# Optimization experiments

Measured on AMD Instinct MI355X. Metric: run time of the kernel, lower is better.

## Reference

```python
import jax, jax.numpy as jnp
import numpy as np

C = 64; NB_ERB = 32; NB_DF = 96; EMB = 256; KT = 2
LSNR_SCALE = 50.0; LSNR_OFFSET = -15.0

def _conv2d(x, w, b, stride=(1, 1)):
    # NCHW conv; freq padding 1, no temporal padding (causal ring buffer handles time)
    out = jax.lax.conv_general_dilated(
        x, w, window_strides=stride, padding=((0, 0), (1, 1)),
        dimension_numbers=('NCHW', 'OIHW', 'NCHW'))
    return out + b[None, :, None, None]


def setup_inputs() -> dict:
    key = jax.random.key(0)
    ks = jax.random.split(key, 32)
    n = lambda i, shape, s=0.05: jax.random.normal(ks[i], shape, dtype=jnp.float32) * s
    return {
        'feat_erb': n(0, (1, 1, 1, NB_ERB), 1.0),
        'feat_spec': n(1, (1, 2, 1, NB_DF), 1.0),
        'buf_erb0': n(2, (1, 1, KT - 1, NB_ERB), 1.0),
        'buf_df0': n(3, (1, 2, KT - 1, NB_DF), 1.0),
        'h_enc': n(4, (1, 1, EMB), 1.0),
        'W_erb0': n(5, (C, 1, KT, 3)), 'b_erb0': n(6, (C,)),
        'W_erb1': n(7, (C, C, 1, 3)), 'b_erb1': n(8, (C,)),
        'W_erb2': n(9, (C, C, 1, 3)), 'b_erb2': n(10, (C,)),
        'W_erb3': n(11, (C, C, 1, 3)), 'b_erb3': n(12, (C,)),
        'W_df0': n(13, (C, 2, KT, 3)), 'b_df0': n(14, (C,)),
        'W_df1': n(15, (C, C, 1, 3)), 'b_df1': n(16, (C,)),
        'W_dffc': n(17, (EMB, C * (NB_DF // 2))), 'b_dffc': n(18, (EMB,)),
        'W_ih': n(19, (3 * EMB, EMB)), 'b_ih': n(20, (3 * EMB,)),
        'W_hh': n(21, (3 * EMB, EMB)), 'b_hh': n(22, (3 * EMB,)),
        'W_lsnr': n(23, (1, EMB)), 'b_lsnr': n(24, (1,)),
    }


def reference(feat_erb, feat_spec, buf_erb0, buf_df0, h_enc,
              W_erb0, b_erb0, W_erb1, b_erb1, W_erb2, b_erb2, W_erb3, b_erb3,
              W_df0, b_df0, W_df1, b_df1, W_dffc, b_dffc,
              W_ih, b_ih, W_hh, b_hh, W_lsnr, b_lsnr):
    relu = jax.nn.relu
    # ERB path: causal conv via explicit ring buffer
    ctx_erb = jnp.concatenate([buf_erb0, feat_erb], axis=2)     # [1,1,KT,32]
    e0 = relu(_conv2d(ctx_erb, W_erb0, b_erb0))                 # [1,C,1,32]
    buf_erb0_new = ctx_erb[:, :, 1:, :]
    e1 = relu(_conv2d(e0, W_erb1, b_erb1, stride=(1, 2)))       # [1,C,1,16]
    e2 = relu(_conv2d(e1, W_erb2, b_erb2, stride=(1, 2)))       # [1,C,1,8]
    e3 = relu(_conv2d(e2, W_erb3, b_erb3, stride=(1, 2)))       # [1,C,1,4]
    # DF path
    ctx_df = jnp.concatenate([buf_df0, feat_spec], axis=2)      # [1,2,KT,96]
    c0 = relu(_conv2d(ctx_df, W_df0, b_df0))                    # [1,C,1,96]
    buf_df0_new = ctx_df[:, :, 1:, :]
    c1 = relu(_conv2d(c0, W_df1, b_df1, stride=(1, 2)))         # [1,C,1,48]
    c1f = jnp.transpose(c1, (0, 2, 3, 1)).reshape(1, 1, -1)     # [1,1,48*C]
    cemb = relu(c1f @ W_dffc.T + b_dffc)                        # [1,1,EMB]
    emb_raw = jnp.transpose(e3, (0, 2, 3, 1)).reshape(1, 1, -1) # [1,1,EMB]
    emb_raw = emb_raw + cemb                                    # combine = add
    # Single-layer GRU step (torch gate semantics)
    x2 = emb_raw[:, 0]                                          # [1,EMB]
    h2 = h_enc[0]                                               # [1,EMB]
    gi = x2 @ W_ih.T + b_ih
    gh = h2 @ W_hh.T + b_hh
    ir, iz, inn = jnp.split(gi, 3, axis=-1)
    hr, hz, hn = jnp.split(gh, 3, axis=-1)
    r = jax.nn.sigmoid(ir + hr)
    z = jax.nn.sigmoid(iz + hz)
    ng = jnp.tanh(inn + r * hn)
    h_new = (1.0 - z) * ng + z * h2                             # [1,EMB]
    emb = h_new[:, None, :]                                     # [1,1,EMB]
    h_enc_new = h_new[None]                                     # [1,1,EMB]
    lsnr = (jax.nn.sigmoid(emb @ W_lsnr.T + b_lsnr) * LSNR_SCALE + LSNR_OFFSET).reshape(1)
    return (e0, e1, e2, e3, emb, c0, lsnr, buf_erb0_new, buf_df0_new, h_enc_new)
```

## Files before the change

### kernel.cpp

```cpp
#include <hip/hip_runtime.h>
#include <math.h>

#define NB_ERB 32
#define NB_DF 96
#define EMB 256

#define OUT_E0      0
#define OUT_E1      2048
#define OUT_E2      3072
#define OUT_E3      3584
#define OUT_EMB     3840
#define OUT_C0      4096
#define OUT_LSNR    10240
#define OUT_BUF_ERB 10241
#define OUT_BUF_DF  10273
#define OUT_HENC    10465

#define WS_GH   0
#define WS_PART 768

static __device__ __forceinline__ float sigm(float x) {
    return 1.0f / (1.0f + expf(-x));
}

__global__ __launch_bounds__(256) void k1(
    const float* __restrict__ feat_erb, const float* __restrict__ feat_spec,
    const float* __restrict__ buf_erb0, const float* __restrict__ buf_df0,
    const float* __restrict__ h_enc,
    const float* __restrict__ W_erb0, const float* __restrict__ b_erb0,
    const float* __restrict__ W_df0,  const float* __restrict__ b_df0,
    const float* __restrict__ W_hh,   const float* __restrict__ b_hh,
    float* __restrict__ out, float* __restrict__ ws)
{
    const int blk = blockIdx.x, t = threadIdx.x;
    if (blk < 24) {
        int g = blk * 256 + t;
        int o = g / NB_DF, w = g % NB_DF;
        float acc = b_df0[o];
        const float* W = W_df0 + o * 12;
        #pragma unroll
        for (int c = 0; c < 2; ++c)
            #pragma unroll
            for (int kw = 0; kw < 3; ++kw) {
                int x = w + kw - 1;
                if (x >= 0 && x < NB_DF) {
                    acc += W[c * 6 + kw]     * buf_df0[c * NB_DF + x];
                    acc += W[c * 6 + 3 + kw] * feat_spec[c * NB_DF + x];
                }
            }
        out[OUT_C0 + g] = fmaxf(acc, 0.0f);
    } else if (blk < 32) {
        int g = (blk - 24) * 256 + t;
        int o = g / NB_ERB, w = g % NB_ERB;
        float acc = b_erb0[o];
        const float* W = W_erb0 + o * 6;
        #pragma unroll
        for (int kw = 0; kw < 3; ++kw) {
            int x = w + kw - 1;
            if (x >= 0 && x < NB_ERB) {
                acc += W[kw]     * buf_erb0[x];
                acc += W[3 + kw] * feat_erb[x];
            }
        }
        out[OUT_E0 + g] = fmaxf(acc, 0.0f);
    } else if (blk < 80) {
        const int wv = t >> 6, lane = t & 63;
        const int o0 = (blk - 32) * 16 + wv * 4;
        const float4 hv = *reinterpret_cast<const float4*>(h_enc + lane * 4);
        float r[4];
        #pragma unroll
        for (int j = 0; j < 4; ++j) {
            const float4 wr = *reinterpret_cast<const float4*>(W_hh + (o0 + j) * EMB + lane * 4);
            r[j] = wr.x * hv.x + wr.y * hv.y + wr.z * hv.z + wr.w * hv.w;
        }
        #pragma unroll
        for (int off = 32; off; off >>= 1) {
            #pragma unroll
            for (int j = 0; j < 4; ++j) r[j] += __shfl_down(r[j], off);
        }
        if (lane == 0) {
            #pragma unroll
            for (int j = 0; j < 4; ++j) ws[WS_GH + o0 + j] = r[j] + b_hh[o0 + j];
        }
    } else {
        if (t < 32)  out[OUT_BUF_ERB + t] = feat_erb[t];
        if (t < 192) out[OUT_BUF_DF + t]  = feat_spec[t];
    }
}

__global__ __launch_bounds__(256) void k2(
    const float* __restrict__ W_erb1, const float* __restrict__ b_erb1,
    const float* __restrict__ W_erb2, const float* __restrict__ b_erb2,
    const float* __restrict__ W_erb3, const float* __restrict__ b_erb3,
    const float* __restrict__ W_df1,  const float* __restrict__ b_df1,
    const float* __restrict__ W_dffc,
    float* __restrict__ out, float* __restrict__ ws)
{
    const int blk = blockIdx.x, t = threadIdx.x;
    __shared__ float sW1[64 * 193];
    __shared__ float sW2[64 * 193];
    __shared__ __align__(16) float sA[2048];
    __shared__ __align__(16) float sB[1024];
    __shared__ float s_c0[192];
    __shared__ float s_c1[64];

    if (blk == 0) {
        const int o = t & 63, wg = t >> 6;
        float4 wbuf[12];

        {
            const float4* W1v = reinterpret_cast<const float4*>(W_erb1);
            #pragma unroll
            for (int j = 0; j < 12; ++j) wbuf[j] = W1v[t + 256 * j];
            const float4* e0v = reinterpret_cast<const float4*>(out + OUT_E0);
            float4 a0 = e0v[t], a1 = e0v[t + 256];
            reinterpret_cast<float4*>(sA)[t]       = a0;
            reinterpret_cast<float4*>(sA)[t + 256] = a1;
            #pragma unroll
            for (int j = 0; j < 12; ++j) {
                int k4 = t + 256 * j;
                float* p = &sW1[(k4 / 48) * 193 + (k4 % 48) * 4];
                p[0] = wbuf[j].x; p[1] = wbuf[j].y; p[2] = wbuf[j].z; p[3] = wbuf[j].w;
            }
            const float4* W2v = reinterpret_cast<const float4*>(W_erb2);
            #pragma unroll
            for (int j = 0; j < 12; ++j) wbuf[j] = W2v[t + 256 * j];
        }
        __syncthreads();

        {
            float bias = b_erb1[o];
            float a0 = bias, a1 = bias, a2 = bias, a3 = bias;
            const float* wrow = &sW1[o * 193];
            for (int i = 0; i < 64; ++i) {
                float w0 = wrow[i * 3], w1 = wrow[i * 3 + 1], w2 = wrow[i * 3 + 2];
                const float* e = &sA[i * 32 + wg * 8];
                float em1 = (wg == 0) ? 0.0f : e[-1];
                float4 v0 = *reinterpret_cast<const float4*>(e);
                float4 v1 = *reinterpret_cast<const float4*>(e + 4);
                a0 += w0 * em1  + w1 * v0.x + w2 * v0.y;
                a1 += w0 * v0.y + w1 * v0.z + w2 * v0.w;
                a2 += w0 * v0.w + w1 * v1.x + w2 * v1.y;
                a3 += w0 * v1.y + w1 * v1.z + w2 * v1.w;
            }
            float4 r = make_float4(fmaxf(a0, 0.f), fmaxf(a1, 0.f),
                                   fmaxf(a2, 0.f), fmaxf(a3, 0.f));
            reinterpret_cast<float4*>(&sB[o * 16])[wg] = r;
            reinterpret_cast<float4*>(out + OUT_E1)[o * 4 + wg] = r;
        }
        {
            #pragma unroll
            for (int j = 0; j < 12; ++j) {
                int k4 = t + 256 * j;
                float* p = &sW2[(k4 / 48) * 193 + (k4 % 48) * 4];
                p[0] = wbuf[j].x; p[1] = wbuf[j].y; p[2] = wbuf[j].z; p[3] = wbuf[j].w;
            }
            const float4* W3v = reinterpret_cast<const float4*>(W_erb3);
            #pragma unroll
            for (int j = 0; j < 12; ++j) wbuf[j] = W3v[t + 256 * j];
        }
        __syncthreads();

        {
            float bias = b_erb2[o];
            float a0 = bias, a1 = bias;
            const float* wrow = &sW2[o * 193];
            for (int i = 0; i < 64; ++i) {
                float w0 = wrow[i * 3], w1 = wrow[i * 3 + 1], w2 = wrow[i * 3 + 2];
                const float* e = &sB[i * 16 + wg * 4];
                float em1 = (wg == 0) ? 0.0f : e[-1];
                float4 v = *reinterpret_cast<const float4*>(e);
                a0 += w0 * em1 + w1 * v.x + w2 * v.y;
                a1 += w0 * v.y + w1 * v.z + w2 * v.w;
            }
            a0 = fmaxf(a0, 0.0f); a1 = fmaxf(a1, 0.0f);
            int w = 2 * wg;
            sA[o * 8 + w] = a0; sA[o * 8 + w + 1] = a1;
            out[OUT_E2 + o * 8 + w] = a0; out[OUT_E2 + o * 8 + w + 1] = a1;
        }
        {
            #pragma unroll
            for (int j = 0; j < 12; ++j) {
                int k4 = t + 256 * j;
                float* p = &sW1[(k4 / 48) * 193 + (k4 % 48) * 4];
                p[0] = wbuf[j].x; p[1] = wbuf[j].y; p[2] = wbuf[j].z; p[3] = wbuf[j].w;
            }
        }
        __syncthreads();

        {
            float a = b_erb3[o];
            const float* wrow = &sW1[o * 193];
            for (int i = 0; i < 64; ++i) {
                float w0 = wrow[i * 3], w1 = wrow[i * 3 + 1], w2 = wrow[i * 3 + 2];
                const float* e = &sA[i * 8 + 2 * wg];
                float em1 = (wg == 0) ? 0.0f : e[-1];
                a += w0 * em1 + w1 * e[0] + w2 * e[1];
            }
            out[OUT_E3 + o * 4 + wg] = fmaxf(a, 0.0f);
        }
    } else {
        const int w = blk - 1;
        const float* c0p = out + OUT_C0;
        if (t < 192) {
            int i = t / 3, kw = t % 3, x = 2 * w + kw - 1;
            s_c0[t] = (x >= 0) ? c0p[i * NB_DF + x] : 0.0f;
        }
        __syncthreads();
        const int c = t >> 2, p = t & 3;
        float wloc[48];
        {
            const float4* Wv = reinterpret_cast<const float4*>(W_df1 + c * 192 + p * 48);
            #pragma unroll
            for (int q = 0; q < 12; ++q) {
                float4 v = Wv[q];
                wloc[4 * q] = v.x; wloc[4 * q + 1] = v.y;
                wloc[4 * q + 2] = v.z; wloc[4 * q + 3] = v.w;
            }
        }
        float acc = 0.0f;
        #pragma unroll
        for (int ii = 0; ii < 16; ++ii) {
            int i = p * 16 + ii;
            acc += wloc[ii * 3]     * s_c0[i * 3]
                 + wloc[ii * 3 + 1] * s_c0[i * 3 + 1]
                 + wloc[ii * 3 + 2] * s_c0[i * 3 + 2];
        }
        acc += __shfl_down(acc, 2, 4);
        acc += __shfl_down(acc, 1, 4);
        if (p == 0) s_c1[c] = fmaxf(acc + b_df1[c], 0.0f);
        __syncthreads();
        {
            const float4* Wp = reinterpret_cast<const float4*>(W_dffc + t * 3072 + w * 64);
            float a = 0.0f;
            #pragma unroll
            for (int q = 0; q < 16; ++q) {
                float4 v = Wp[q];
                a += v.x * s_c1[q * 4]     + v.y * s_c1[q * 4 + 1]
                   + v.z * s_c1[q * 4 + 2] + v.w * s_c1[q * 4 + 3];
            }
            ws[WS_PART + w * 256 + t] = a;
        }
    }
}

__global__ __launch_bounds__(256) void k3(
    const float* __restrict__ h_enc, const float* __restrict__ b_dffc,
    const float* __restrict__ W_ih,  const float* __restrict__ b_ih,
    float* __restrict__ out, float* __restrict__ ws)
{
    const int t = threadIdx.x, blk = blockIdx.x;
    __shared__ __align__(16) float s_x2[256];
    {
        float acc = b_dffc[t];
        #pragma unroll 8
        for (int w = 0; w < 48; ++w) acc += ws[WS_PART + w * 256 + t];
        float cemb = fmaxf(acc, 0.0f);
        float e3v = out[OUT_E3 + (t & 63) * 4 + (t >> 6)];
        s_x2[t] = e3v + cemb;
    }
    __syncthreads();
    const int wv = t >> 6, lane = t & 63;
    const int o = blk * 4 + wv;
    const float4 xv = *reinterpret_cast<const float4*>(&s_x2[lane * 4]);
    const float4 wr = *reinterpret_cast<const float4*>(W_ih + (o      ) * EMB + lane * 4);
    const float4 wz = *reinterpret_cast<const float4*>(W_ih + (o + 256) * EMB + lane * 4);
    const float4 wn = *reinterpret_cast<const float4*>(W_ih + (o + 512) * EMB + lane * 4);
    float ar = wr.x * xv.x + wr.y * xv.y + wr.z * xv.z + wr.w * xv.w;
    float az = wz.x * xv.x + wz.y * xv.y + wz.z * xv.z + wz.w * xv.w;
    float an = wn.x * xv.x + wn.y * xv.y + wn.z * xv.z + wn.w * xv.w;
    #pragma unroll
    for (int off = 32; off; off >>= 1) {
        ar += __shfl_down(ar, off);
        az += __shfl_down(az, off);
        an += __shfl_down(an, off);
    }
    if (lane == 0) {
        float r  = sigm(ar + b_ih[o]       + ws[WS_GH + o]);
        float z  = sigm(az + b_ih[o + 256] + ws[WS_GH + 256 + o]);
        float ng = tanhf(an + b_ih[o + 512] + r * ws[WS_GH + 512 + o]);
        float h  = (1.0f - z) * ng + z * h_enc[o];
        out[OUT_EMB  + o] = h;
        out[OUT_HENC + o] = h;
    }
}

__global__ __launch_bounds__(256) void k4(
    const float* __restrict__ W_lsnr, const float* __restrict__ b_lsnr,
    float* __restrict__ out)
{
    const int t = threadIdx.x;
    __shared__ float s[4];
    float v = out[OUT_EMB + t] * W_lsnr[t];
    #pragma unroll
    for (int off = 32; off; off >>= 1) v += __shfl_down(v, off);
    if ((t & 63) == 0) s[t >> 6] = v;
    __syncthreads();
    if (t == 0)
        out[OUT_LSNR] = sigm(s[0] + s[1] + s[2] + s[3] + b_lsnr[0]) * 50.0f - 15.0f;
}

extern "C" void kernel_launch(void* const* d_in, const int* in_sizes, int n_in,
                              void* d_out, int out_size, void* d_ws, size_t ws_size,
                              hipStream_t stream) {
    (void)in_sizes; (void)n_in; (void)out_size; (void)ws_size;
    const float* feat_erb  = (const float*)d_in[0];
    const float* feat_spec = (const float*)d_in[1];
    const float* buf_erb0  = (const float*)d_in[2];
    const float* buf_df0   = (const float*)d_in[3];
    const float* h_enc     = (const float*)d_in[4];
    const float* W_erb0    = (const float*)d_in[5];
    const float* b_erb0    = (const float*)d_in[6];
    const float* W_erb1    = (const float*)d_in[7];
    const float* b_erb1    = (const float*)d_in[8];
    const float* W_erb2    = (const float*)d_in[9];
    const float* b_erb2    = (const float*)d_in[10];
    const float* W_erb3    = (const float*)d_in[11];
    const float* b_erb3    = (const float*)d_in[12];
    const float* W_df0     = (const float*)d_in[13];
    const float* b_df0     = (const float*)d_in[14];
    const float* W_df1     = (const float*)d_in[15];
    const float* b_df1     = (const float*)d_in[16];
    const float* W_dffc    = (const float*)d_in[17];
    const float* b_dffc    = (const float*)d_in[18];
    const float* W_ih      = (const float*)d_in[19];
    const float* b_ih      = (const float*)d_in[20];
    const float* W_hh      = (const float*)d_in[21];
    const float* b_hh      = (const float*)d_in[22];
    const float* W_lsnr    = (const float*)d_in[23];
    const float* b_lsnr    = (const float*)d_in[24];
    float* out = (float*)d_out;
    float* ws  = (float*)d_ws;

    hipLaunchKernelGGL(k1, dim3(81), dim3(256), 0, stream,
                       feat_erb, feat_spec, buf_erb0, buf_df0, h_enc,
                       W_erb0, b_erb0, W_df0, b_df0, W_hh, b_hh, out, ws);
    hipLaunchKernelGGL(k2, dim3(49), dim3(256), 0, stream,
                       W_erb1, b_erb1, W_erb2, b_erb2, W_erb3, b_erb3,
                       W_df1, b_df1, W_dffc, out, ws);
    hipLaunchKernelGGL(k3, dim3(64), dim3(256), 0, stream,
                       h_enc, b_dffc, W_ih, b_ih, out, ws);
    hipLaunchKernelGGL(k4, dim3(1), dim3(256), 0, stream,
                       W_lsnr, b_lsnr, out);
}
```

Measured before the change: 126.0 us.

## Fuse first-layer convs into conv stack kernel and GH matvec into GRU kernel

Removes the first kernel. The ERB first conv is now computed inside block 0 of the conv-stack kernel and written straight to shared memory. The DF first conv is recomputed per output column (with its halo) inside each DF block. The W_hh matvec moves into the GRU kernel alongside W_ih, so the launch chain drops from four kernels to three and there is no gh round-trip through workspace. In exchange there is some redundant DF conv0 recomputation at block boundaries, and a longer critical path in block 0 before its weights land in shared memory.

```diff
diff --git a/kernel.cpp b/kernel.cpp
--- a/kernel.cpp
+++ b/kernel.cpp
@@ -16,82 +16,20 @@
 #define OUT_BUF_DF  10273
 #define OUT_HENC    10465
 
-#define WS_GH   0
-#define WS_PART 768
+#define WS_PART 0
 
 static __device__ __forceinline__ float sigm(float x) {
     return 1.0f / (1.0f + expf(-x));
 }
 
-__global__ __launch_bounds__(256) void k1(
+__global__ __launch_bounds__(256) void ka(
     const float* __restrict__ feat_erb, const float* __restrict__ feat_spec,
     const float* __restrict__ buf_erb0, const float* __restrict__ buf_df0,
-    const float* __restrict__ h_enc,
     const float* __restrict__ W_erb0, const float* __restrict__ b_erb0,
-    const float* __restrict__ W_df0,  const float* __restrict__ b_df0,
-    const float* __restrict__ W_hh,   const float* __restrict__ b_hh,
-    float* __restrict__ out, float* __restrict__ ws)
-{
-    const int blk = blockIdx.x, t = threadIdx.x;
-    if (blk < 24) {
-        int g = blk * 256 + t;
-        int o = g / NB_DF, w = g % NB_DF;
-        float acc = b_df0[o];
-        const float* W = W_df0 + o * 12;
-        #pragma unroll
-        for (int c = 0; c < 2; ++c)
-            #pragma unroll
-            for (int kw = 0; kw < 3; ++kw) {
-                int x = w + kw - 1;
-                if (x >= 0 && x < NB_DF) {
-                    acc += W[c * 6 + kw]     * buf_df0[c * NB_DF + x];
-                    acc += W[c * 6 + 3 + kw] * feat_spec[c * NB_DF + x];
-                }
-            }
-        out[OUT_C0 + g] = fmaxf(acc, 0.0f);
-    } else if (blk < 32) {
-        int g = (blk - 24) * 256 + t;
-        int o = g / NB_ERB, w = g % NB_ERB;
-        float acc = b_erb0[o];
-        const float* W = W_erb0 + o * 6;
-        #pragma unroll
-        for (int kw = 0; kw < 3; ++kw) {
-            int x = w + kw - 1;
-            if (x >= 0 && x < NB_ERB) {
-                acc += W[kw]     * buf_erb0[x];
-                acc += W[3 + kw] * feat_erb[x];
-            }
-        }
-        out[OUT_E0 + g] = fmaxf(acc, 0.0f);
-    } else if (blk < 80) {
-        const int wv = t >> 6, lane = t & 63;
-        const int o0 = (blk - 32) * 16 + wv * 4;
-        const float4 hv = *reinterpret_cast<const float4*>(h_enc + lane * 4);
-        float r[4];
-        #pragma unroll
-        for (int j = 0; j < 4; ++j) {
-            const float4 wr = *reinterpret_cast<const float4*>(W_hh + (o0 + j) * EMB + lane * 4);
-            r[j] = wr.x * hv.x + wr.y * hv.y + wr.z * hv.z + wr.w * hv.w;
-        }
-        #pragma unroll
-        for (int off = 32; off; off >>= 1) {
-            #pragma unroll
-            for (int j = 0; j < 4; ++j) r[j] += __shfl_down(r[j], off);
-        }
-        if (lane == 0) {
-            #pragma unroll
-            for (int j = 0; j < 4; ++j) ws[WS_GH + o0 + j] = r[j] + b_hh[o0 + j];
-        }
-    } else {
-        if (t < 32)  out[OUT_BUF_ERB + t] = feat_erb[t];
-        if (t < 192) out[OUT_BUF_DF + t]  = feat_spec[t];
-    }
-}
-
-__global__ __launch_bounds__(256) void k2(
     const float* __restrict__ W_erb1, const float* __restrict__ b_erb1,
     const float* __restrict__ W_erb2, const float* __restrict__ b_erb2,
     const float* __restrict__ W_erb3, const float* __restrict__ b_erb3,
+    const float* __restrict__ W_df0,  const float* __restrict__ b_df0,
     const float* __restrict__ W_df1,  const float* __restrict__ b_df1,
     const float* __restrict__ W_dffc,
     float* __restrict__ out, float* __restrict__ ws)
@@ -112,10 +50,28 @@
             const float4* W1v = reinterpret_cast<const float4*>(W_erb1);
             #pragma unroll
             for (int j = 0; j < 12; ++j) wbuf[j] = W1v[t + 256 * j];
-            const float4* e0v = reinterpret_cast<const float4*>(out + OUT_E0);
-            float4 a0 = e0v[t], a1 = e0v[t + 256];
-            reinterpret_cast<float4*>(sA)[t]       = a0;
-            reinterpret_cast<float4*>(sA)[t + 256] = a1;
+        }
+        {
+            const int oc = t >> 2, q = t & 3;
+            const float* W = W_erb0 + oc * 6;
+            const float b0 = b_erb0[oc];
+            #pragma unroll
+            for (int m = 0; m < 8; ++m) {
+                int w_ = q * 8 + m;
+                float a = b0;
+                #pragma unroll
+                for (int kw = 0; kw < 3; ++kw) {
+                    int x = w_ + kw - 1;
+                    if (x >= 0 && x < NB_ERB)
+                        a += W[kw] * buf_erb0[x] + W[3 + kw] * feat_erb[x];
+                }
+                float v = fmaxf(a, 0.0f);
+                sA[oc * 32 + w_] = v;
+                out[OUT_E0 + oc * 32 + w_] = v;
+            }
+        }
+        if (t < 32) out[OUT_BUF_ERB + t] = feat_erb[t];
+        {
             #pragma unroll
             for (int j = 0; j < 12; ++j) {
                 int k4 = t + 256 * j;
@@ -201,10 +157,28 @@
         }
     } else {
         const int w = blk - 1;
-        const float* c0p = out + OUT_C0;
+        if (blk == 1 && t < 192) out[OUT_BUF_DF + t] = feat_spec[t];
         if (t < 192) {
-            int i = t / 3, kw = t % 3, x = 2 * w + kw - 1;
-            s_c0[t] = (x >= 0) ? c0p[i * NB_DF + x] : 0.0f;
+            const int i = t & 63, j = t >> 6;
+            const int X = 2 * w - 1 + j;
+            float v = 0.0f;
+            if (X >= 0) {
+                float acc = b_df0[i];
+                const float* Wp = W_df0 + i * 12;
+                #pragma unroll
+                for (int c = 0; c < 2; ++c)
+                    #pragma unroll
+                    for (int kw = 0; kw < 3; ++kw) {
+                        int x = X + kw - 1;
+                        if (x >= 0 && x < NB_DF) {
+                            acc += Wp[c * 6 + kw]     * buf_df0[c * NB_DF + x];
+                            acc += Wp[c * 6 + 3 + kw] * feat_spec[c * NB_DF + x];
+                        }
+                    }
+                v = fmaxf(acc, 0.0f);
+                if (j >= 1) out[OUT_C0 + i * NB_DF + X] = v;
+            }
+            s_c0[i * 3 + j] = v;
         }
         __syncthreads();
         const int c = t >> 2, p = t & 3;
@@ -244,10 +218,11 @@
     }
 }
 
-__global__ __launch_bounds__(256) void k3(
+__global__ __launch_bounds__(256) void kb(
     const float* __restrict__ h_enc, const float* __restrict__ b_dffc,
     const float* __restrict__ W_ih,  const float* __restrict__ b_ih,
-    float* __restrict__ out, float* __restrict__ ws)
+    const float* __restrict__ W_hh,  const float* __restrict__ b_hh,
+    float* __restrict__ out, const float* __restrict__ ws)
 {
     const int t = threadIdx.x, blk = blockIdx.x;
     __shared__ __align__(16) float s_x2[256];
@@ -263,29 +238,39 @@
     const int wv = t >> 6, lane = t & 63;
     const int o = blk * 4 + wv;
     const float4 xv = *reinterpret_cast<const float4*>(&s_x2[lane * 4]);
-    const float4 wr = *reinterpret_cast<const float4*>(W_ih + (o      ) * EMB + lane * 4);
-    const float4 wz = *reinterpret_cast<const float4*>(W_ih + (o + 256) * EMB + lane * 4);
-    const float4 wn = *reinterpret_cast<const float4*>(W_ih + (o + 512) * EMB + lane * 4);
-    float ar = wr.x * xv.x + wr.y * xv.y + wr.z * xv.z + wr.w * xv.w;
-    float az = wz.x * xv.x + wz.y * xv.y + wz.z * xv.z + wz.w * xv.w;
-    float an = wn.x * xv.x + wn.y * xv.y + wn.z * xv.z + wn.w * xv.w;
+    const float4 hv = *reinterpret_cast<const float4*>(h_enc + lane * 4);
+    const float4 wir = *reinterpret_cast<const float4*>(W_ih + (o      ) * EMB + lane * 4);
+    const float4 wiz = *reinterpret_cast<const float4*>(W_ih + (o + 256) * EMB + lane * 4);
+    const float4 win = *reinterpret_cast<const float4*>(W_ih + (o + 512) * EMB + lane * 4);
+    const float4 whr = *reinterpret_cast<const float4*>(W_hh + (o      ) * EMB + lane * 4);
+    const float4 whz = *reinterpret_cast<const float4*>(W_hh + (o + 256) * EMB + lane * 4);
+    const float4 whn = *reinterpret_cast<const float4*>(W_hh + (o + 512) * EMB + lane * 4);
+    float air = wir.x * xv.x + wir.y * xv.y + wir.z * xv.z + wir.w * xv.w;
+    float aiz = wiz.x * xv.x + wiz.y * xv.y + wiz.z * xv.z + wiz.w * xv.w;
+    float ain = win.x * xv.x + win.y * xv.y + win.z * xv.z + win.w * xv.w;
+    float ahr = whr.x * hv.x + whr.y * hv.y + whr.z * hv.z + whr.w * hv.w;
+    float ahz = whz.x * hv.x + whz.y * hv.y + whz.z * hv.z + whz.w * hv.w;
+    float ahn = whn.x * hv.x + whn.y * hv.y + whn.z * hv.z + whn.w * hv.w;
     #pragma unroll
     for (int off = 32; off; off >>= 1) {
-        ar += __shfl_down(ar, off);
-        az += __shfl_down(az, off);
-        an += __shfl_down(an, off);
+        air += __shfl_down(air, off);
+        aiz += __shfl_down(aiz, off);
+        ain += __shfl_down(ain, off);
+        ahr += __shfl_down(ahr, off);
+        ahz += __shfl_down(ahz, off);
+        ahn += __shfl_down(ahn, off);
     }
     if (lane == 0) {
-        float r  = sigm(ar + b_ih[o]       + ws[WS_GH + o]);
-        float z  = sigm(az + b_ih[o + 256] + ws[WS_GH + 256 + o]);
-        float ng = tanhf(an + b_ih[o + 512] + r * ws[WS_GH + 512 + o]);
+        float r  = sigm(air + b_ih[o]       + ahr + b_hh[o]);
+        float z  = sigm(aiz + b_ih[o + 256] + ahz + b_hh[o + 256]);
+        float ng = tanhf(ain + b_ih[o + 512] + r * (ahn + b_hh[o + 512]));
         float h  = (1.0f - z) * ng + z * h_enc[o];
         out[OUT_EMB  + o] = h;
         out[OUT_HENC + o] = h;
     }
 }
 
-__global__ __launch_bounds__(256) void k4(
+__global__ __launch_bounds__(256) void kc(
     const float* __restrict__ W_lsnr, const float* __restrict__ b_lsnr,
     float* __restrict__ out)
 {
@@ -332,14 +317,13 @@
     float* out = (float*)d_out;
     float* ws  = (float*)d_ws;
 
-    hipLaunchKernelGGL(k1, dim3(81), dim3(256), 0, stream,
-                       feat_erb, feat_spec, buf_erb0, buf_df0, h_enc,
-                       W_erb0, b_erb0, W_df0, b_df0, W_hh, b_hh, out, ws);
-    hipLaunchKernelGGL(k2, dim3(49), dim3(256), 0, stream,
-                       W_erb1, b_erb1, W_erb2, b_erb2, W_erb3, b_erb3,
-                       W_df1, b_df1, W_dffc, out, ws);
-    hipLaunchKernelGGL(k3, dim3(64), dim3(256), 0, stream,
-                       h_enc, b_dffc, W_ih, b_ih, out, ws);
-    hipLaunchKernelGGL(k4, dim3(1), dim3(256), 0, stream,
+    hipLaunchKernelGGL(ka, dim3(49), dim3(256), 0, stream,
+                       feat_erb, feat_spec, buf_erb0, buf_df0,
+                       W_erb0, b_erb0, W_erb1, b_erb1, W_erb2, b_erb2,
+                       W_erb3, b_erb3, W_df0, b_df0, W_df1, b_df1,
+                       W_dffc, out, ws);
+    hipLaunchKernelGGL(kb, dim3(64), dim3(256), 0, stream,
+                       h_enc, b_dffc, W_ih, b_ih, W_hh, b_hh, out, ws);
+    hipLaunchKernelGGL(kc, dim3(1), dim3(256), 0, stream,
                        W_lsnr, b_lsnr, out);
 }
```

Measured after the change: 125.1 us, median of 2. No clear change (-0.7%).
